# Kernel optimization log

Hardware: AMD Instinct MI355X
Metric: run time of the kernel (lower is better)

## Reference

```python
import jax, jax.numpy as jnp
import numpy as np
from jax import lax

B, L, C, P = 512, 6, 4, 45

def _conv(x, w, b, pad):
    y = lax.conv_general_dilated(x, w, (1, 1), [(pad, pad), (pad, pad)],
                                 dimension_numbers=('NCHW', 'OIHW', 'NCHW'))
    return y + b[None, :, None, None]

def _maxpool2(x):
    return lax.reduce_window(x, -jnp.inf, lax.max, (1, 1, 2, 2), (1, 1, 2, 2), 'VALID')

def _prelu(x, a):
    return jnp.where(x >= 0, x, a * x)

def setup_inputs() -> dict:
    key = jax.random.key(0)
    ks = jax.random.split(key, 16)
    s = 0.05
    inp = {
        'x': jax.random.normal(ks[0], (B, L, C, P, P), jnp.float32),
        'w0': jax.random.normal(ks[1], (32, C, 5, 5), jnp.float32) * s,
        'b0': jnp.zeros((32,), jnp.float32),
        'w1': jax.random.normal(ks[2], (32, 32, 5, 5), jnp.float32) * s,
        'b1': jnp.zeros((32,), jnp.float32),
        'w2': jax.random.normal(ks[3], (64, 32, 4, 4), jnp.float32) * s,
        'b2': jnp.zeros((64,), jnp.float32),
        'w3': jax.random.normal(ks[4], (64, 64, 3, 3), jnp.float32) * s,
        'b3': jnp.zeros((64,), jnp.float32),
        'a0': jnp.float32(0.25), 'a1': jnp.float32(0.25),
        'a2': jnp.float32(0.25), 'a3': jnp.float32(0.25),
        'fc1_w': jax.random.normal(ks[5], (L, 256, 128), jnp.float32) * s,
        'fc1_b': jnp.zeros((L, 128), jnp.float32),
        'a4': jnp.full((L, 1), 0.25, jnp.float32),
        'fc2_w': jax.random.normal(ks[6], (L, 128, 64), jnp.float32) * s,
        'fc2_b': jnp.zeros((L, 64), jnp.float32),
        'a5': jnp.full((L, 1), 0.25, jnp.float32),
        'fc3_w': jax.random.normal(ks[7], (L, 64, 4), jnp.float32) * s,
        'fc3_b': jnp.zeros((L, 4), jnp.float32),
    }
    return inp

def reference(x, w0, b0, w1, b1, w2, b2, w3, b3, a0, a1, a2, a3,
              fc1_w, fc1_b, a4, fc2_w, fc2_b, a5, fc3_w, fc3_b):
    b, l = x.shape[0], x.shape[1]
    # Conv tower shares weights across landmarks -> fold landmark into batch.
    h = x.reshape(b * l, x.shape[2], P, P)
    h = _maxpool2(_prelu(_conv(h, w0, b0, 1), a0))   # (BL,32,21,21)
    h = _maxpool2(_prelu(_conv(h, w1, b1, 1), a1))   # (BL,32,9,9)
    h = _maxpool2(_prelu(_conv(h, w2, b2, 1), a2))   # (BL,64,4,4)
    h = _prelu(_conv(h, w3, b3, 0), a3)              # (BL,64,2,2)
    h = h.reshape(b, l, 256)
    # Per-landmark FC heads as batched GEMMs.
    h = _prelu(jnp.einsum('bli,lio->blo', h, fc1_w) + fc1_b, a4)
    h = _prelu(jnp.einsum('bli,lio->blo', h, fc2_w) + fc2_b, a5)
    out = jnp.einsum('bli,lio->blo', h, fc3_w) + fc3_b   # (B,L,4)
    return out
```

## Files before the change

### kernel.cpp

```cpp
#include <hip/hip_runtime.h>
#include <stdint.h>

typedef _Float16 f16;
typedef _Float16 half8 __attribute__((ext_vector_type(8)));
typedef _Float16 half4 __attribute__((ext_vector_type(4)));
typedef float floatx16 __attribute__((ext_vector_type(16)));

#define NIMG 3072

#define WS_W0T   0
#define WS_W1T   10240
#define WS_W2T   61440
#define WS_W3T   126976
#define WS_FC1T  200704
#define WS_FC2T  593920
#define WS_FC3T  692224
#define WS_H2    720896
#define WS_H3F   16646144

#define Z16 {0.f,0.f,0.f,0.f,0.f,0.f,0.f,0.f,0.f,0.f,0.f,0.f,0.f,0.f,0.f,0.f}

__global__ __launch_bounds__(256) void k_prep(
    const float* __restrict__ w0, const float* __restrict__ w1, const float* __restrict__ w2,
    const float* __restrict__ w3, const float* __restrict__ fc1w, const float* __restrict__ fc2w,
    const float* __restrict__ fc3w,
    f16* __restrict__ w0t, f16* __restrict__ w1t, f16* __restrict__ w2t, f16* __restrict__ w3t,
    f16* __restrict__ fc1t, f16* __restrict__ fc2t, f16* __restrict__ fc3t)
{
  int stride = gridDim.x * blockDim.x;
  int g0 = blockIdx.x * blockDim.x + threadIdx.x;
  for (int i = g0; i < 5120; i += stride) {
    int j = i & 7, co = (i >> 3) & 31, hf = (i >> 8) & 1, ch = (i >> 9) & 1, ky = i >> 10;
    int k = ch * 16 + hf * 8 + j;
    f16 v = (f16)0.f;
    if (k < 20) { int kx = k >> 2, ci = k & 3; v = (f16)w0[((co * 4 + ci) * 5 + ky) * 5 + kx]; }
    w0t[i] = v;
  }
  for (int i = g0; i < 25600; i += stride) {
    int j = i & 7, co = (i >> 3) & 31, hf = (i >> 8) & 1, ch = (i >> 9) & 1, tap = i >> 10;
    int ci = ch * 16 + hf * 8 + j, ky = tap / 5, kx = tap % 5;
    w1t[i] = (f16)w1[((co * 32 + ci) * 5 + ky) * 5 + kx];
  }
  for (int i = g0; i < 32768; i += stride) {
    int j = i & 7, co = (i >> 3) & 31, hf = (i >> 8) & 1, ct = (i >> 9) & 1, ch = (i >> 10) & 1, tap = i >> 11;
    int ci = ch * 16 + hf * 8 + j, cog = ct * 32 + co, ky = tap >> 2, kx = tap & 3;
    w2t[i] = (f16)w2[((cog * 32 + ci) * 4 + ky) * 4 + kx];
  }
  for (int i = g0; i < 36864; i += stride) {
    int j = i & 7, col = (i >> 3) & 31, hf = (i >> 8) & 1, ct = (i >> 9) & 1, c = i >> 10;
    int k = c * 16 + hf * 8 + j, tap = k >> 6, ci = k & 63, co = ct * 32 + col;
    int ky = tap / 3, kx = tap % 3;
    w3t[i] = (f16)w3[((co * 64 + ci) * 3 + ky) * 3 + kx];
  }
  for (int i = g0; i < 196608; i += stride) {
    int j = i & 7, col = (i >> 3) & 31, hf = (i >> 8) & 1, nt = (i >> 9) & 3, c = (i >> 11) & 15, l = i >> 15;
    int k = c * 16 + hf * 8 + j, o = nt * 32 + col;
    fc1t[i] = (f16)fc1w[(l * 256 + k) * 128 + o];
  }
  for (int i = g0; i < 49152; i += stride) {
    int j = i & 7, col = (i >> 3) & 31, hf = (i >> 8) & 1, nt = (i >> 9) & 1, c = (i >> 10) & 7, l = i >> 13;
    int k = c * 16 + hf * 8 + j, o = nt * 32 + col;
    fc2t[i] = (f16)fc2w[(l * 128 + k) * 64 + o];
  }
  for (int i = g0; i < 12288; i += stride) {
    int j = i & 7, col = (i >> 3) & 31, hf = (i >> 8) & 1, c = (i >> 9) & 3, l = i >> 11;
    int k = c * 16 + hf * 8 + j;
    f16 v = (f16)0.f;
    if (col < 4) v = (f16)fc3w[(l * 64 + k) * 4 + col];
    fc3t[i] = v;
  }
}

__global__ __launch_bounds__(512) void k_conv01(
    const float* __restrict__ x,
    const f16* __restrict__ w0t, const float* __restrict__ b0, const float* __restrict__ a0p,
    const f16* __restrict__ w1t, const float* __restrict__ b1, const float* __restrict__ a1p,
    f16* __restrict__ h2g)
{
  __shared__ __align__(16) uint32_t smem_u[16328];
  f16* sh   = (f16*)smem_u;
  f16* s_x  = sh;
  f16* s_h1 = sh + 9776;

  const int n = blockIdx.x, tid = threadIdx.x;
  const int wv = tid >> 6, l = tid & 63;
  const int hf = l >> 5, m = l & 31, dr = m >> 3, dc = m & 7, col = m;
  const float a0 = a0p[0], a1 = a1p[0];
  const float b0c = b0[col], b1c = b1[col];
  const half8* w0t8 = (const half8*)w0t;
  const half8* w1t8 = (const half8*)w1t;

  for (int i = tid; i < 16328; i += 512) smem_u[i] = 0u;
  __syncthreads();
  const float* xin = x + n * 8100;
  for (int i = tid; i < 8100; i += 512) {
    int ci = i / 2025, r = i % 2025;
    int y = r / 45, xx = r % 45;
    s_x[((y + 1) * 52 + (xx + 1)) * 4 + ci] = (f16)xin[i];
  }
  __syncthreads();

  half8 B0[5][2];
  #pragma unroll
  for (int ky = 0; ky < 5; ++ky)
    #pragma unroll
    for (int ch = 0; ch < 2; ++ch)
      B0[ky][ch] = w0t8[(ky * 2 + ch) * 64 + hf * 32 + col];

  const int r0lut0[11] = {0,4,8,12,16,20,24,28,32,36,38};
  for (int t = wv; t < 66; t += 8) {
    int r0 = r0lut0[t / 6], cb = (t % 6) * 8;
    int rowb = r0 + dr, colb = cb + dc;
    const f16* pA0 = s_x + (rowb * 52 + colb + 2 * hf) * 4;
    const f16* pA1 = s_x + (rowb * 52 + colb + 4) * 4;
    floatx16 acc = Z16;
    #pragma unroll
    for (int ky = 0; ky < 5; ++ky) {
      half4 lo = *(const half4*)(pA0 + ky * 208);
      half4 hi = *(const half4*)(pA0 + ky * 208 + 4);
      half8 a0v = __builtin_shufflevector(lo, hi, 0,1,2,3,4,5,6,7);
      acc = __builtin_amdgcn_mfma_f32_32x32x16_f16(a0v, B0[ky][0], acc, 0, 0, 0);
      half8 a1v = {(f16)0,(f16)0,(f16)0,(f16)0,(f16)0,(f16)0,(f16)0,(f16)0};
      if (hf == 0) {
        half4 l1 = *(const half4*)(pA1 + ky * 208);
        a1v[0] = l1[0]; a1v[1] = l1[1]; a1v[2] = l1[2]; a1v[3] = l1[3];
      }
      acc = __builtin_amdgcn_mfma_f32_32x32x16_f16(a1v, B0[ky][1], acc, 0, 0, 0);
    }
    #pragma unroll
    for (int pp = 0; pp < 2; ++pp)
      #pragma unroll
      for (int c2 = 0; c2 < 2; ++c2) {
        float v = fmaxf(fmaxf(acc[8*pp + 2*c2], acc[8*pp + 2*c2 + 1]),
                        fmaxf(acc[8*pp + 4 + 2*c2], acc[8*pp + 4 + 2*c2 + 1]));
        v += b0c; v = (v >= 0.f) ? v : a0 * v;
        int pr = (r0 >> 1) + pp, pc = (cb >> 1) + 2 * hf + c2;
        if (pc < 21) s_h1[((pr + 1) * 26 + (pc + 1)) * 40 + col] = (f16)v;
      }
  }
  __syncthreads();

  const int r0lut1[5] = {0, 4, 8, 12, 14};
  const int cclut[3]  = {0, 8, 14};
  int t0 = wv * 2;
  int t1 = t0 + 1; if (t1 > 14) t1 = 14;
  int r0a = r0lut1[t0 / 3], cca = cclut[t0 % 3];
  int r0b = r0lut1[t1 / 3], ccb = cclut[t1 % 3];
  const f16* pAa = s_h1 + ((r0a + dr) * 26 + cca + dc) * 40 + hf * 8;
  const f16* pAb = s_h1 + ((r0b + dr) * 26 + ccb + dc) * 40 + hf * 8;
  floatx16 accA = Z16;
  floatx16 accB = Z16;
  for (int ky = 0; ky < 5; ++ky) {
    const half8* wb = w1t8 + ky * 640 + hf * 32 + col;
    const f16* qa = pAa + ky * 1040;
    const f16* qb = pAb + ky * 1040;
    #pragma unroll
    for (int kx = 0; kx < 5; ++kx) {
      #pragma unroll
      for (int ch = 0; ch < 2; ++ch) {
        half8 b  = wb[kx * 128 + ch * 64];
        half8 aA = *(const half8*)(qa + kx * 40 + ch * 16);
        half8 aB = *(const half8*)(qb + kx * 40 + ch * 16);
        accA = __builtin_amdgcn_mfma_f32_32x32x16_f16(aA, b, accA, 0, 0, 0);
        accB = __builtin_amdgcn_mfma_f32_32x32x16_f16(aB, b, accB, 0, 0, 0);
      }
    }
  }
  f16* outp = h2g + n * 2592;
  #pragma unroll
  for (int tt = 0; tt < 2; ++tt) {
    const floatx16 acc = tt ? accB : accA;
    int r0 = tt ? r0b : r0a, cc = tt ? ccb : cca;
    #pragma unroll
    for (int pp = 0; pp < 2; ++pp)
      #pragma unroll
      for (int c2 = 0; c2 < 2; ++c2) {
        float v = fmaxf(fmaxf(acc[8*pp + 2*c2], acc[8*pp + 2*c2 + 1]),
                        fmaxf(acc[8*pp + 4 + 2*c2], acc[8*pp + 4 + 2*c2 + 1]));
        v += b1c; v = (v >= 0.f) ? v : a1 * v;
        int pr = (r0 >> 1) + pp, pc = (cc >> 1) + 2 * hf + c2;
        if (pc < 9) outp[(pr * 9 + pc) * 32 + col] = (f16)v;
      }
  }
}

__global__ __launch_bounds__(256) void k_conv2(
    const f16* __restrict__ h2g, const f16* __restrict__ w2t,
    const float* __restrict__ b2, const float* __restrict__ a2p,
    f16* __restrict__ h3f)
{
  __shared__ __align__(16) uint32_t s_u[5760];
  f16* s2 = (f16*)s_u;
  const int n0 = blockIdx.x * 2, tid = threadIdx.x;
  const int wv = tid >> 6, l = tid & 63;
  const int hf = l >> 5, m = l & 31, dr = m >> 3, dc = m & 7, col = m;
  const int img = wv >> 1, ct = wv & 1;
  const float a2 = a2p[0];
  const float b2c = b2[ct * 32 + col];
  const half8* w2t8 = (const half8*)w2t;

  for (int i = tid; i < 5760; i += 256) s_u[i] = 0u;
  __syncthreads();
  for (int c = tid; c < 648; c += 256) {
    int im = c / 324, rr = c % 324, pos = rr >> 2, part = rr & 3;
    int r = pos / 9, cc = pos % 9;
    *(half8*)(s2 + im * 5760 + ((r + 1) * 12 + (cc + 1)) * 40 + part * 8) =
      *(const half8*)(h2g + (n0 + im) * 2592 + pos * 32 + part * 8);
  }
  __syncthreads();

  const f16* sbase = s2 + img * 5760;
  const f16* pA0 = sbase + (dr * 12 + dc) * 40 + hf * 8;
  const f16* pA4 = sbase + ((4 + dr) * 12 + dc) * 40 + hf * 8;
  floatx16 acc0 = Z16;
  floatx16 acc4 = Z16;
  for (int tap = 0; tap < 16; ++tap) {
    int ky = tap >> 2, kx = tap & 3;
    int aoff = (ky * 12 + kx) * 40;
    #pragma unroll
    for (int ch = 0; ch < 2; ++ch) {
      half8 b  = w2t8[tap * 256 + ch * 128 + ct * 64 + hf * 32 + col];
      half8 a0 = *(const half8*)(pA0 + aoff + ch * 16);
      half8 a4 = *(const half8*)(pA4 + aoff + ch * 16);
      acc0 = __builtin_amdgcn_mfma_f32_32x32x16_f16(a0, b, acc0, 0, 0, 0);
      acc4 = __builtin_amdgcn_mfma_f32_32x32x16_f16(a4, b, acc4, 0, 0, 0);
    }
  }
  f16* o = h3f + (n0 + img) * 1024;
  #pragma unroll
  for (int tt = 0; tt < 2; ++tt) {
    const floatx16 acc = tt ? acc4 : acc0;
    #pragma unroll
    for (int pp = 0; pp < 2; ++pp)
      #pragma unroll
      for (int c2 = 0; c2 < 2; ++c2) {
        float v = fmaxf(fmaxf(acc[8*pp + 2*c2], acc[8*pp + 2*c2 + 1]),
                        fmaxf(acc[8*pp + 4 + 2*c2], acc[8*pp + 4 + 2*c2 + 1]));
        v += b2c; v = (v >= 0.f) ? v : a2 * v;
        int pr = tt * 2 + pp, pc = 2 * hf + c2, co = ct * 32 + col;
        o[(pr * 4 + pc) * 64 + co] = (f16)v;
      }
  }
}

__global__ __launch_bounds__(256) void k_tail(
    const f16* __restrict__ h3f,
    const f16* __restrict__ w3t, const float* __restrict__ b3, const float* __restrict__ a3p,
    const f16* __restrict__ fc1t, const float* __restrict__ fc1b, const float* __restrict__ a4,
    const f16* __restrict__ fc2t, const float* __restrict__ fc2b, const float* __restrict__ a5,
    const f16* __restrict__ fc3t, const float* __restrict__ fc3b,
    float* __restrict__ out)
{
  __shared__ __align__(16) f16 s_feat[32 * 264];
  __shared__ __align__(16) f16 s_g1[32 * 136];
  __shared__ __align__(16) f16 s_g2[32 * 72];

  const int lm = blockIdx.x % 6, t = blockIdx.x / 6;
  const int tid = threadIdx.x, wv = tid >> 6, lane = tid & 63;
  const int hf = lane >> 5, col = lane & 31;
  const half8* w3t8  = (const half8*)w3t;
  const half8* fc1t8 = (const half8*)fc1t;
  const half8* fc2t8 = (const half8*)fc2t;
  const half8* fc3t8 = (const half8*)fc3t;

  {
    const int mt = wv;
    const int i_img = mt * 8 + (col >> 2);
    const int pos = col & 3, oy = pos >> 1, ox = pos & 1;
    const int gimg = (t * 32 + i_img) * 6 + lm;
    const f16* Abase = h3f + gimg * 1024 + (oy * 4 + ox) * 64;
    floatx16 acc0 = Z16, acc1 = Z16;
    for (int c = 0; c < 36; ++c) {
      int tap = c >> 2;
      int ky = tap / 3, kx = tap % 3;
      half8 a = *(const half8*)(Abase + (ky * 4 + kx) * 64 + (c & 3) * 16 + hf * 8);
      half8 bb0 = w3t8[((c * 2 + 0) * 2 + hf) * 32 + col];
      half8 bb1 = w3t8[((c * 2 + 1) * 2 + hf) * 32 + col];
      acc0 = __builtin_amdgcn_mfma_f32_32x32x16_f16(a, bb0, acc0, 0, 0, 0);
      acc1 = __builtin_amdgcn_mfma_f32_32x32x16_f16(a, bb1, acc1, 0, 0, 0);
    }
    const float a3 = a3p[0];
    #pragma unroll
    for (int ct = 0; ct < 2; ++ct) {
      const floatx16 acc = ct ? acc1 : acc0;
      const int co = ct * 32 + col;
      const float bb = b3[co];
      #pragma unroll
      for (int q = 0; q < 4; ++q) {
        int ii = mt * 8 + 2 * q + hf;
        half4 w;
        #pragma unroll
        for (int z = 0; z < 4; ++z) {
          float v = acc[q * 4 + z] + bb;
          v = (v >= 0.f) ? v : a3 * v;
          w[z] = (f16)v;
        }
        *(half4*)(s_feat + ii * 264 + co * 4) = w;
      }
    }
  }
  __syncthreads();

  {
    floatx16 g = Z16;
    for (int c = 0; c < 16; ++c) {
      half8 a = *(const half8*)(s_feat + col * 264 + c * 16 + hf * 8);
      half8 b = fc1t8[(((lm * 16 + c) * 4 + wv) * 2 + hf) * 32 + col];
      g = __builtin_amdgcn_mfma_f32_32x32x16_f16(a, b, g, 0, 0, 0);
    }
    const float a4v = a4[lm];
    const float bb = fc1b[lm * 128 + wv * 32 + col];
    #pragma unroll
    for (int reg = 0; reg < 16; ++reg) {
      int r = (reg & 3) + 8 * (reg >> 2) + 4 * hf;
      float v = g[reg] + bb;
      v = (v >= 0.f) ? v : a4v * v;
      s_g1[r * 136 + wv * 32 + col] = (f16)v;
    }
  }
  __syncthreads();

  if (wv < 2) {
    floatx16 g = Z16;
    for (int c = 0; c < 8; ++c) {
      half8 a = *(const half8*)(s_g1 + col * 136 + c * 16 + hf * 8);
      half8 b = fc2t8[(((lm * 8 + c) * 2 + wv) * 2 + hf) * 32 + col];
      g = __builtin_amdgcn_mfma_f32_32x32x16_f16(a, b, g, 0, 0, 0);
    }
    const float a5v = a5[lm];
    const float bb = fc2b[lm * 64 + wv * 32 + col];
    #pragma unroll
    for (int reg = 0; reg < 16; ++reg) {
      int r = (reg & 3) + 8 * (reg >> 2) + 4 * hf;
      float v = g[reg] + bb;
      v = (v >= 0.f) ? v : a5v * v;
      s_g2[r * 72 + wv * 32 + col] = (f16)v;
    }
  }
  __syncthreads();

  if (wv == 0) {
    floatx16 g = Z16;
    for (int c = 0; c < 4; ++c) {
      half8 a = *(const half8*)(s_g2 + col * 72 + c * 16 + hf * 8);
      half8 b = fc3t8[((lm * 4 + c) * 2 + hf) * 32 + col];
      g = __builtin_amdgcn_mfma_f32_32x32x16_f16(a, b, g, 0, 0, 0);
    }
    if (col < 4) {
      const float bb = fc3b[lm * 4 + col];
      #pragma unroll
      for (int reg = 0; reg < 16; ++reg) {
        int r = (reg & 3) + 8 * (reg >> 2) + 4 * hf;
        out[((t * 32 + r) * 6 + lm) * 4 + col] = g[reg] + bb;
      }
    }
  }
}

extern "C" void kernel_launch(void* const* d_in, const int* in_sizes, int n_in,
                              void* d_out, int out_size, void* d_ws, size_t ws_size,
                              hipStream_t stream) {
  const float* x    = (const float*)d_in[0];
  const float* w0   = (const float*)d_in[1];
  const float* b0   = (const float*)d_in[2];
  const float* w1   = (const float*)d_in[3];
  const float* b1   = (const float*)d_in[4];
  const float* w2   = (const float*)d_in[5];
  const float* b2   = (const float*)d_in[6];
  const float* w3   = (const float*)d_in[7];
  const float* b3   = (const float*)d_in[8];
  const float* a0   = (const float*)d_in[9];
  const float* a1   = (const float*)d_in[10];
  const float* a2   = (const float*)d_in[11];
  const float* a3   = (const float*)d_in[12];
  const float* fc1w = (const float*)d_in[13];
  const float* fc1b = (const float*)d_in[14];
  const float* a4   = (const float*)d_in[15];
  const float* fc2w = (const float*)d_in[16];
  const float* fc2b = (const float*)d_in[17];
  const float* a5   = (const float*)d_in[18];
  const float* fc3w = (const float*)d_in[19];
  const float* fc3b = (const float*)d_in[20];
  float* out = (float*)d_out;

  char* ws = (char*)d_ws;
  f16* w0t  = (f16*)(ws + WS_W0T);
  f16* w1t  = (f16*)(ws + WS_W1T);
  f16* w2t  = (f16*)(ws + WS_W2T);
  f16* w3t  = (f16*)(ws + WS_W3T);
  f16* fc1t = (f16*)(ws + WS_FC1T);
  f16* fc2t = (f16*)(ws + WS_FC2T);
  f16* fc3t = (f16*)(ws + WS_FC3T);
  f16* h2g  = (f16*)(ws + WS_H2);
  f16* h3f  = (f16*)(ws + WS_H3F);

  k_prep  <<<128, 256, 0, stream>>>(w0, w1, w2, w3, fc1w, fc2w, fc3w,
                                    w0t, w1t, w2t, w3t, fc1t, fc2t, fc3t);
  k_conv01<<<NIMG, 512, 0, stream>>>(x, w0t, b0, a0, w1t, b1, a1, h2g);
  k_conv2 <<<NIMG/2, 256, 0, stream>>>(h2g, w2t, b2, a2, h3f);
  k_tail  <<<96, 256, 0, stream>>>(h3f, w3t, b3, a3, fc1t, fc1b, a4,
                                   fc2t, fc2b, a5, fc3t, fc3b, out);
}
```

Baseline: 342.7 us.

## Fuse conv2 into conv0/1 kernel, keeping conv1 output in shared memory

Merges the separate conv2 kernel into the conv0+conv1 kernel so that the pooled conv1 activations stay in LDS (reusing the input buffer region) rather than being written to and re-read from global memory, and one launch is removed. The input load is rewritten to gather all four channels per pixel and store them as one half4, and the conv0 row/column mapping is permuted so that each 2x2 pooling window sits in four consecutive accumulator elements. Conv2 runs on only 4 of the 8 waves per image, which adds serial work at the end of every block and leaves half the block idle during that phase.

```diff
diff --git a/kernel.cpp b/kernel.cpp
--- a/kernel.cpp
+++ b/kernel.cpp
@@ -15,7 +15,6 @@
 #define WS_FC1T  200704
 #define WS_FC2T  593920
 #define WS_FC3T  692224
-#define WS_H2    720896
 #define WS_H3F   16646144
 
 #define Z16 {0.f,0.f,0.f,0.f,0.f,0.f,0.f,0.f,0.f,0.f,0.f,0.f,0.f,0.f,0.f,0.f}
@@ -71,11 +70,12 @@
   }
 }
 
-__global__ __launch_bounds__(512) void k_conv01(
+__global__ __launch_bounds__(512) void k_conv012(
     const float* __restrict__ x,
     const f16* __restrict__ w0t, const float* __restrict__ b0, const float* __restrict__ a0p,
     const f16* __restrict__ w1t, const float* __restrict__ b1, const float* __restrict__ a1p,
-    f16* __restrict__ h2g)
+    const f16* __restrict__ w2t, const float* __restrict__ b2, const float* __restrict__ a2p,
+    f16* __restrict__ h3f)
 {
   __shared__ __align__(16) uint32_t smem_u[16328];
   f16* sh   = (f16*)smem_u;
@@ -89,14 +89,19 @@
   const float b0c = b0[col], b1c = b1[col];
   const half8* w0t8 = (const half8*)w0t;
   const half8* w1t8 = (const half8*)w1t;
+  const half8* w2t8 = (const half8*)w2t;
 
   for (int i = tid; i < 16328; i += 512) smem_u[i] = 0u;
   __syncthreads();
   const float* xin = x + n * 8100;
-  for (int i = tid; i < 8100; i += 512) {
-    int ci = i / 2025, r = i % 2025;
-    int y = r / 45, xx = r % 45;
-    s_x[((y + 1) * 52 + (xx + 1)) * 4 + ci] = (f16)xin[i];
+  for (int p = tid; p < 2025; p += 512) {
+    int y = p / 45, xx = p % 45;
+    half4 h;
+    h[0] = (f16)xin[p];
+    h[1] = (f16)xin[p + 2025];
+    h[2] = (f16)xin[p + 4050];
+    h[3] = (f16)xin[p + 6075];
+    *(half4*)(s_x + ((y + 1) * 52 + (xx + 1)) * 4) = h;
   }
   __syncthreads();
 
@@ -107,10 +112,13 @@
     for (int ch = 0; ch < 2; ++ch)
       B0[ky][ch] = w0t8[(ky * 2 + ch) * 64 + hf * 32 + col];
 
-  const int r0lut0[11] = {0,4,8,12,16,20,24,28,32,36,38};
+  const int cdr = (m & 1) | ((m & 8) >> 2);
+  const int cdc = ((m >> 1) & 3) | ((m & 16) >> 2);
   for (int t = wv; t < 66; t += 8) {
-    int r0 = r0lut0[t / 6], cb = (t % 6) * 8;
-    int rowb = r0 + dr, colb = cb + dc;
+    int g = t / 6;
+    int r0 = 4 * g; if (r0 > 38) r0 = 38;
+    int cb = (t % 6) * 8;
+    int rowb = r0 + cdr, colb = cb + cdc;
     const f16* pA0 = s_x + (rowb * 52 + colb + 2 * hf) * 4;
     const f16* pA1 = s_x + (rowb * 52 + colb + 4) * 4;
     floatx16 acc = Z16;
@@ -128,24 +136,23 @@
       acc = __builtin_amdgcn_mfma_f32_32x32x16_f16(a1v, B0[ky][1], acc, 0, 0, 0);
     }
     #pragma unroll
-    for (int pp = 0; pp < 2; ++pp)
-      #pragma unroll
-      for (int c2 = 0; c2 < 2; ++c2) {
-        float v = fmaxf(fmaxf(acc[8*pp + 2*c2], acc[8*pp + 2*c2 + 1]),
-                        fmaxf(acc[8*pp + 4 + 2*c2], acc[8*pp + 4 + 2*c2 + 1]));
-        v += b0c; v = (v >= 0.f) ? v : a0 * v;
-        int pr = (r0 >> 1) + pp, pc = (cb >> 1) + 2 * hf + c2;
-        if (pc < 21) s_h1[((pr + 1) * 26 + (pc + 1)) * 40 + col] = (f16)v;
-      }
-  }
-  __syncthreads();
-
-  const int r0lut1[5] = {0, 4, 8, 12, 14};
-  const int cclut[3]  = {0, 8, 14};
+    for (int q = 0; q < 4; ++q) {
+      float v = fmaxf(fmaxf(acc[4*q], acc[4*q + 1]), fmaxf(acc[4*q + 2], acc[4*q + 3]));
+      v += b0c; v = (v >= 0.f) ? v : a0 * v;
+      int pr = (r0 >> 1) + (q & 1), pc = (cb >> 1) + hf + 2 * (q >> 1);
+      if (pc < 21) s_h1[((pr + 1) * 26 + (pc + 1)) * 40 + col] = (f16)v;
+    }
+  }
+  __syncthreads();
+
+  for (int i = tid; i < 2880; i += 512) smem_u[i] = 0u;
+
   int t0 = wv * 2;
   int t1 = t0 + 1; if (t1 > 14) t1 = 14;
-  int r0a = r0lut1[t0 / 3], cca = cclut[t0 % 3];
-  int r0b = r0lut1[t1 / 3], ccb = cclut[t1 % 3];
+  int r0a = 4 * (t0 / 3); if (r0a > 14) r0a = 14;
+  int cca = 8 * (t0 % 3); if (cca > 14) cca = 14;
+  int r0b = 4 * (t1 / 3); if (r0b > 14) r0b = 14;
+  int ccb = 8 * (t1 % 3); if (ccb > 14) ccb = 14;
   const f16* pAa = s_h1 + ((r0a + dr) * 26 + cca + dc) * 40 + hf * 8;
   const f16* pAb = s_h1 + ((r0b + dr) * 26 + ccb + dc) * 40 + hf * 8;
   floatx16 accA = Z16;
@@ -166,7 +173,9 @@
       }
     }
   }
-  f16* outp = h2g + n * 2592;
+  __syncthreads();
+
+  f16* s2 = s_x;
   #pragma unroll
   for (int tt = 0; tt < 2; ++tt) {
     const floatx16 acc = tt ? accB : accA;
@@ -179,57 +188,28 @@
                         fmaxf(acc[8*pp + 4 + 2*c2], acc[8*pp + 4 + 2*c2 + 1]));
         v += b1c; v = (v >= 0.f) ? v : a1 * v;
         int pr = (r0 >> 1) + pp, pc = (cc >> 1) + 2 * hf + c2;
-        if (pc < 9) outp[(pr * 9 + pc) * 32 + col] = (f16)v;
-      }
-  }
-}
-
-__global__ __launch_bounds__(256) void k_conv2(
-    const f16* __restrict__ h2g, const f16* __restrict__ w2t,
-    const float* __restrict__ b2, const float* __restrict__ a2p,
-    f16* __restrict__ h3f)
-{
-  __shared__ __align__(16) uint32_t s_u[5760];
-  f16* s2 = (f16*)s_u;
-  const int n0 = blockIdx.x * 2, tid = threadIdx.x;
-  const int wv = tid >> 6, l = tid & 63;
-  const int hf = l >> 5, m = l & 31, dr = m >> 3, dc = m & 7, col = m;
-  const int img = wv >> 1, ct = wv & 1;
-  const float a2 = a2p[0];
-  const float b2c = b2[ct * 32 + col];
-  const half8* w2t8 = (const half8*)w2t;
-
-  for (int i = tid; i < 5760; i += 256) s_u[i] = 0u;
-  __syncthreads();
-  for (int c = tid; c < 648; c += 256) {
-    int im = c / 324, rr = c % 324, pos = rr >> 2, part = rr & 3;
-    int r = pos / 9, cc = pos % 9;
-    *(half8*)(s2 + im * 5760 + ((r + 1) * 12 + (cc + 1)) * 40 + part * 8) =
-      *(const half8*)(h2g + (n0 + im) * 2592 + pos * 32 + part * 8);
-  }
-  __syncthreads();
-
-  const f16* sbase = s2 + img * 5760;
-  const f16* pA0 = sbase + (dr * 12 + dc) * 40 + hf * 8;
-  const f16* pA4 = sbase + ((4 + dr) * 12 + dc) * 40 + hf * 8;
-  floatx16 acc0 = Z16;
-  floatx16 acc4 = Z16;
-  for (int tap = 0; tap < 16; ++tap) {
-    int ky = tap >> 2, kx = tap & 3;
-    int aoff = (ky * 12 + kx) * 40;
-    #pragma unroll
-    for (int ch = 0; ch < 2; ++ch) {
-      half8 b  = w2t8[tap * 256 + ch * 128 + ct * 64 + hf * 32 + col];
-      half8 a0 = *(const half8*)(pA0 + aoff + ch * 16);
-      half8 a4 = *(const half8*)(pA4 + aoff + ch * 16);
-      acc0 = __builtin_amdgcn_mfma_f32_32x32x16_f16(a0, b, acc0, 0, 0, 0);
-      acc4 = __builtin_amdgcn_mfma_f32_32x32x16_f16(a4, b, acc4, 0, 0, 0);
-    }
-  }
-  f16* o = h3f + (n0 + img) * 1024;
-  #pragma unroll
-  for (int tt = 0; tt < 2; ++tt) {
-    const floatx16 acc = tt ? acc4 : acc0;
+        if (pc < 9) s2[((pr + 1) * 12 + (pc + 1)) * 40 + col] = (f16)v;
+      }
+  }
+  __syncthreads();
+
+  if (wv < 4) {
+    const int mt = wv >> 1, c2t = wv & 1;
+    const float a2 = a2p[0];
+    const float b2c = b2[c2t * 32 + col];
+    const f16* pA = s2 + ((mt * 4 + dr) * 12 + dc) * 40 + hf * 8;
+    floatx16 acc = Z16;
+    #pragma unroll 4
+    for (int tap = 0; tap < 16; ++tap) {
+      int aoff = ((tap >> 2) * 12 + (tap & 3)) * 40;
+      #pragma unroll
+      for (int ch = 0; ch < 2; ++ch) {
+        half8 b = w2t8[tap * 256 + ch * 128 + c2t * 64 + hf * 32 + col];
+        half8 a = *(const half8*)(pA + aoff + ch * 16);
+        acc = __builtin_amdgcn_mfma_f32_32x32x16_f16(a, b, acc, 0, 0, 0);
+      }
+    }
+    f16* o = h3f + n * 1024;
     #pragma unroll
     for (int pp = 0; pp < 2; ++pp)
       #pragma unroll
@@ -237,8 +217,8 @@
         float v = fmaxf(fmaxf(acc[8*pp + 2*c2], acc[8*pp + 2*c2 + 1]),
                         fmaxf(acc[8*pp + 4 + 2*c2], acc[8*pp + 4 + 2*c2 + 1]));
         v += b2c; v = (v >= 0.f) ? v : a2 * v;
-        int pr = tt * 2 + pp, pc = 2 * hf + c2, co = ct * 32 + col;
-        o[(pr * 4 + pc) * 64 + co] = (f16)v;
+        int pr = mt * 2 + pp, pc = 2 * hf + c2;
+        o[(pr * 4 + pc) * 64 + c2t * 32 + col] = (f16)v;
       }
   }
 }
@@ -391,13 +371,11 @@
   f16* fc1t = (f16*)(ws + WS_FC1T);
   f16* fc2t = (f16*)(ws + WS_FC2T);
   f16* fc3t = (f16*)(ws + WS_FC3T);
-  f16* h2g  = (f16*)(ws + WS_H2);
   f16* h3f  = (f16*)(ws + WS_H3F);
 
-  k_prep  <<<128, 256, 0, stream>>>(w0, w1, w2, w3, fc1w, fc2w, fc3w,
-                                    w0t, w1t, w2t, w3t, fc1t, fc2t, fc3t);
-  k_conv01<<<NIMG, 512, 0, stream>>>(x, w0t, b0, a0, w1t, b1, a1, h2g);
-  k_conv2 <<<NIMG/2, 256, 0, stream>>>(h2g, w2t, b2, a2, h3f);
-  k_tail  <<<96, 256, 0, stream>>>(h3f, w3t, b3, a3, fc1t, fc1b, a4,
-                                   fc2t, fc2b, a5, fc3t, fc3b, out);
+  k_prep   <<<128, 256, 0, stream>>>(w0, w1, w2, w3, fc1w, fc2w, fc3w,
+                                     w0t, w1t, w2t, w3t, fc1t, fc2t, fc3t);
+  k_conv012<<<NIMG, 512, 0, stream>>>(x, w0t, b0, a0, w1t, b1, a1, w2t, b2, a2, h3f);
+  k_tail   <<<96, 256, 0, stream>>>(h3f, w3t, b3, a3, fc1t, fc1b, a4,
+                                    fc2t, fc2b, a5, fc3t, fc3b, out);
 }
```

Result: faster. 328.1 us (-4.3%).
